# Optimization experiments

Hardware: AMD Instinct MI355X
Metric: run time of the kernel (lower is better)

The kernel has to match this reference:

```python
import jax, jax.numpy as jnp
import numpy as np

B, S, D, H, F = 8, 1024, 1024, 16, 4096
HD = D // H
SCALING = HD ** -0.5
EPS = 1e-5


def layer_norm(x, g, b):
    m = jnp.mean(x, axis=-1, keepdims=True)
    v = jnp.mean(jnp.square(x - m), axis=-1, keepdims=True)
    return (x - m) * jax.lax.rsqrt(v + EPS) * g + b


def setup_inputs() -> dict:
    key = jax.random.key(0)
    ks = jax.random.split(key, 8)
    std = 0.02
    return {
        "hidden_states": jax.random.normal(ks[0], (B, S, D), jnp.float32),
        "wq": jax.random.normal(ks[1], (D, D), jnp.float32) * std,
        "bq": jnp.zeros((D,), jnp.float32),
        "wk": jax.random.normal(ks[2], (D, D), jnp.float32) * std,
        "bk": jnp.zeros((D,), jnp.float32),
        "wv": jax.random.normal(ks[3], (D, D), jnp.float32) * std,
        "bv": jnp.zeros((D,), jnp.float32),
        "wo": jax.random.normal(ks[4], (D, D), jnp.float32) * std,
        "bo": jnp.zeros((D,), jnp.float32),
        "ln1_g": jnp.ones((D,), jnp.float32),
        "ln1_b": jnp.zeros((D,), jnp.float32),
        "fc1_w": jax.random.normal(ks[5], (F, D), jnp.float32) * std,
        "fc1_b": jnp.zeros((F,), jnp.float32),
        "fc2_w": jax.random.normal(ks[6], (D, F), jnp.float32) * std,
        "fc2_b": jnp.zeros((D,), jnp.float32),
        "ln2_g": jnp.ones((D,), jnp.float32),
        "ln2_b": jnp.zeros((D,), jnp.float32),
    }


def reference(hidden_states, wq, bq, wk, bk, wv, bv, wo, bo,
              ln1_g, ln1_b, fc1_w, fc1_b, fc2_w, fc2_b, ln2_g, ln2_b):
    hs = hidden_states
    residual = hs
    # --- manual multi-head self-attention (queries pre-scaled as in source) ---
    q = (hs @ wq.T + bq) * SCALING          # [B,S,D]
    k = hs @ wk.T + bk
    v = hs @ wv.T + bv
    q = q.reshape(B, S, H, HD).transpose(0, 2, 1, 3)  # [B,H,S,HD]
    k = k.reshape(B, S, H, HD).transpose(0, 2, 1, 3)
    v = v.reshape(B, S, H, HD).transpose(0, 2, 1, 3)
    scores = jnp.einsum("bhqd,bhkd->bhqk", q, k)      # [B,H,S,S]
    probs = jax.nn.softmax(scores, axis=-1)
    attn = jnp.einsum("bhqk,bhkd->bhqd", probs, v)    # [B,H,S,HD]
    attn = attn.transpose(0, 2, 1, 3).reshape(B, S, D)
    attn = attn @ wo.T + bo
    hs = layer_norm(residual + attn, ln1_g, ln1_b)
    # --- FFN ---
    residual = hs
    h = jax.nn.gelu(hs @ fc1_w.T + fc1_b, approximate=False)  # [B,S,F]
    h = h @ fc2_w.T + fc2_b
    hs = layer_norm(residual + h, ln2_g, ln2_b)
    return hs
```

## Files before the change

### kernel.cpp

```cpp
#include <hip/hip_runtime.h>
#include <hip/hip_bf16.h>
#include <math.h>

#define B_  8
#define S_  1024
#define D_  1024
#define H_  16
#define HD_ 64
#define F_  4096
#define NROWS_ (B_*S_)
#define SCALING_ 0.125f
#define EPS_ 1e-5f

typedef __attribute__((ext_vector_type(8))) short bf16x8;
typedef __attribute__((ext_vector_type(4))) float f32x4;
typedef __attribute__((ext_vector_type(4))) unsigned short us4;

__device__ __forceinline__ unsigned short f2bf(float f) {
    union { float f; unsigned int u; } x; x.f = f;
    unsigned int u = x.u;
    u += 0x7FFFu + ((u >> 16) & 1u);
    return (unsigned short)(u >> 16);
}

__device__ __forceinline__ f32x4 mfma16(bf16x8 a, bf16x8 b, f32x4 c) {
    return __builtin_amdgcn_mfma_f32_16x16x32_bf16(a, b, c, 0, 0, 0);
}

__device__ __forceinline__ void async_copy16(const unsigned short* g, unsigned short* l) {
    __builtin_amdgcn_global_load_lds(
        (const __attribute__((address_space(1))) void*)g,
        (__attribute__((address_space(3))) void*)l,
        16, 0, 0);
}

__device__ __forceinline__ bf16x8 ld_swz(const unsigned short* lds, int row, int k) {
    const int kg = (k >> 3) ^ (row & 7);
    return *reinterpret_cast<const bf16x8*>(lds + row * 64 + kg * 8);
}

__global__ __launch_bounds__(256)
void cvt_kernel(const float* __restrict__ in, unsigned short* __restrict__ out, int n4) {
    int i = blockIdx.x * 256 + threadIdx.x;
    if (i >= n4) return;
    const float4 v = reinterpret_cast<const float4*>(in)[i];
    us4 o = { f2bf(v.x), f2bf(v.y), f2bf(v.z), f2bf(v.w) };
    reinterpret_cast<us4*>(out)[i] = o;
}

template<int MODE>
__global__ __launch_bounds__(256)
void gemm_bt(const unsigned short* __restrict__ A,
             const unsigned short* __restrict__ Bw,
             const float* __restrict__ bias,
             const float* __restrict__ resid,
             float* __restrict__ outf,
             unsigned short* __restrict__ outb,
             float scale, int M, int N, int K)
{
    alignas(16) __shared__ unsigned short lA[128 * 64];
    alignas(16) __shared__ unsigned short lB[128 * 64];
    const int tid  = threadIdx.x;
    const int lane = tid & 63, wave = tid >> 6;
    const int wr = wave >> 1, wc = wave & 1;
    const int l15 = lane & 15, lg = lane >> 4;
    const int brow = blockIdx.y * 128, bcol = blockIdx.x * 128;

    f32x4 acc[4][4];
#pragma unroll
    for (int m = 0; m < 4; ++m)
#pragma unroll
        for (int n = 0; n < 4; ++n) acc[m][n] = f32x4{0.f, 0.f, 0.f, 0.f};

    for (int k0 = 0; k0 < K; k0 += 64) {
#pragma unroll
        for (int j = 0; j < 4; ++j) {
            const int c   = wave * 4 + j;
            const int p   = c * 64 + lane;
            const int row = p >> 3;
            const int kg  = (p & 7) ^ (row & 7);
            async_copy16(&A [(size_t)(brow + row) * K + k0 + kg * 8], &lA[c * 512]);
            async_copy16(&Bw[(size_t)(bcol + row) * K + k0 + kg * 8], &lB[c * 512]);
        }
        __syncthreads();
#pragma unroll
        for (int kk = 0; kk < 2; ++kk) {
            bf16x8 af[4], bfr[4];
#pragma unroll
            for (int m = 0; m < 4; ++m) af[m]  = ld_swz(lA, wr * 64 + m * 16 + l15, kk * 32 + lg * 8);
#pragma unroll
            for (int n = 0; n < 4; ++n) bfr[n] = ld_swz(lB, wc * 64 + n * 16 + l15, kk * 32 + lg * 8);
#pragma unroll
            for (int m = 0; m < 4; ++m)
#pragma unroll
                for (int n = 0; n < 4; ++n)
                    acc[m][n] = mfma16(af[m], bfr[n], acc[m][n]);
        }
        __syncthreads();
    }

#pragma unroll
    for (int m = 0; m < 4; ++m) {
#pragma unroll
        for (int n = 0; n < 4; ++n) {
#pragma unroll
            for (int r = 0; r < 4; ++r) {
                const int grow = brow + wr * 64 + m * 16 + lg * 4 + r;
                const int gcol = bcol + wc * 64 + n * 16 + l15;
                float v = acc[m][n][r] + bias[gcol];
                if constexpr (MODE == 0) {
                    v *= scale;
                    const int b = grow >> 10, s = grow & 1023, h = gcol >> 6, hd = gcol & 63;
                    outb[(((size_t)b * H_ + h) * S_ + s) * HD_ + hd] = f2bf(v);
                } else if constexpr (MODE == 1) {
                    const int b = grow >> 10, s = grow & 1023, h = gcol >> 6, hd = gcol & 63;
                    outb[(((size_t)b * H_ + h) * HD_ + hd) * S_ + s] = f2bf(v);
                } else if constexpr (MODE == 2 || MODE == 4) {
                    outf[(size_t)grow * N + gcol] = v + resid[(size_t)grow * N + gcol];
                } else {
                    float g = 0.5f * v * (1.0f + erff(v * 0.70710678118654752f));
                    outb[(size_t)grow * N + gcol] = f2bf(g);
                }
            }
        }
    }
}

__global__ __launch_bounds__(256)
void attn_kernel(const unsigned short* __restrict__ qb,
                 const unsigned short* __restrict__ kb,
                 const unsigned short* __restrict__ vtb,
                 unsigned short* __restrict__ attn)
{
    alignas(16) __shared__ unsigned short lK[64 * 64];
    alignas(16) __shared__ unsigned short lV[64 * 64];
    alignas(16) __shared__ unsigned short lP[4][16 * 72];
    const int bh = blockIdx.x, qblk = blockIdx.y;
    const int tid = threadIdx.x, lane = tid & 63, wave = tid >> 6;
    const int l15 = lane & 15, lg = lane >> 4;
    const int b = bh >> 4, h = bh & 15;

    const unsigned short* Kg = kb  + (size_t)bh * S_ * HD_;
    const unsigned short* Vg = vtb + (size_t)bh * HD_ * S_;
    const unsigned short* Qg = qb  + ((size_t)bh * S_ + qblk * 64 + wave * 16) * HD_;

    bf16x8 qf0 = *reinterpret_cast<const bf16x8*>(Qg + l15 * HD_ + lg * 8);
    bf16x8 qf1 = *reinterpret_cast<const bf16x8*>(Qg + l15 * HD_ + lg * 8 + 32);

    float mr[4], lr[4];
    f32x4 o[4];
#pragma unroll
    for (int r = 0; r < 4; ++r) { mr[r] = -1e30f; lr[r] = 0.f; }
#pragma unroll
    for (int n = 0; n < 4; ++n) o[n] = f32x4{0.f, 0.f, 0.f, 0.f};

    for (int t = 0; t < 16; ++t) {
#pragma unroll
        for (int j = 0; j < 2; ++j) {
            const int c   = wave * 2 + j;
            const int p   = c * 64 + lane;
            const int row = p >> 3;
            const int kg  = (p & 7) ^ (row & 7);
            async_copy16(&Kg[(size_t)(t * 64 + row) * HD_ + kg * 8], &lK[c * 512]);
            async_copy16(&Vg[(size_t)row * S_ + t * 64 + kg * 8],    &lV[c * 512]);
        }
        __syncthreads();

        f32x4 sf[4];
#pragma unroll
        for (int n = 0; n < 4; ++n) {
            f32x4 z = {0.f, 0.f, 0.f, 0.f};
            z     = mfma16(qf0, ld_swz(lK, n * 16 + l15, lg * 8), z);
            sf[n] = mfma16(qf1, ld_swz(lK, n * 16 + l15, 32 + lg * 8), z);
        }

        float tmax[4], corr[4], psum[4];
#pragma unroll
        for (int r = 0; r < 4; ++r)
            tmax[r] = fmaxf(fmaxf(sf[0][r], sf[1][r]), fmaxf(sf[2][r], sf[3][r]));
#pragma unroll
        for (int off = 1; off < 16; off <<= 1)
#pragma unroll
            for (int r = 0; r < 4; ++r) tmax[r] = fmaxf(tmax[r], __shfl_xor(tmax[r], off, 64));
#pragma unroll
        for (int r = 0; r < 4; ++r) {
            float mnew = fmaxf(mr[r], tmax[r]);
            corr[r] = __expf(mr[r] - mnew);
            mr[r] = mnew;
            psum[r] = 0.f;
        }
        unsigned short pbf[4][4];
#pragma unroll
        for (int n = 0; n < 4; ++n)
#pragma unroll
            for (int r = 0; r < 4; ++r) {
                float p = __expf(sf[n][r] - mr[r]);
                psum[r] += p;
                pbf[n][r] = f2bf(p);
            }
#pragma unroll
        for (int off = 1; off < 16; off <<= 1)
#pragma unroll
            for (int r = 0; r < 4; ++r) psum[r] += __shfl_xor(psum[r], off, 64);
#pragma unroll
        for (int r = 0; r < 4; ++r) lr[r] = lr[r] * corr[r] + psum[r];
#pragma unroll
        for (int n = 0; n < 4; ++n)
#pragma unroll
            for (int r = 0; r < 4; ++r) o[n][r] *= corr[r];

        unsigned short* Pl = &lP[wave][0];
#pragma unroll
        for (int n = 0; n < 4; ++n)
#pragma unroll
            for (int r = 0; r < 4; ++r)
                Pl[(lg * 4 + r) * 72 + n * 16 + l15] = pbf[n][r];
        asm volatile("s_waitcnt lgkmcnt(0)" ::: "memory");
        __builtin_amdgcn_sched_barrier(0);

#pragma unroll
        for (int kk = 0; kk < 2; ++kk) {
            bf16x8 pf = *reinterpret_cast<const bf16x8*>(Pl + l15 * 72 + kk * 32 + lg * 8);
#pragma unroll
            for (int n = 0; n < 4; ++n)
                o[n] = mfma16(pf, ld_swz(lV, n * 16 + l15, kk * 32 + lg * 8), o[n]);
        }
        __syncthreads();
    }

#pragma unroll
    for (int n = 0; n < 4; ++n)
#pragma unroll
        for (int r = 0; r < 4; ++r) {
            const int s = qblk * 64 + wave * 16 + lg * 4 + r;
            const int d = h * HD_ + n * 16 + l15;
            attn[((size_t)b * S_ + s) * D_ + d] = f2bf(o[n][r] / lr[r]);
        }
}

__global__ __launch_bounds__(256)
void ln_kernel(const float* __restrict__ in, const float* __restrict__ gam,
               const float* __restrict__ bet,
               float* __restrict__ outf, unsigned short* __restrict__ outbf)
{
    const int row = blockIdx.x, t = threadIdx.x;
    const float4 v = reinterpret_cast<const float4*>(in + (size_t)row * D_)[t];
    float s  = v.x + v.y + v.z + v.w;
    float s2 = v.x * v.x + v.y * v.y + v.z * v.z + v.w * v.w;
#pragma unroll
    for (int off = 32; off > 0; off >>= 1) {
        s  += __shfl_down(s, off, 64);
        s2 += __shfl_down(s2, off, 64);
    }
    __shared__ float red[2][4];
    if ((t & 63) == 0) { red[0][t >> 6] = s; red[1][t >> 6] = s2; }
    __syncthreads();
    s  = red[0][0] + red[0][1] + red[0][2] + red[0][3];
    s2 = red[1][0] + red[1][1] + red[1][2] + red[1][3];
    const float mean = s * (1.0f / D_);
    const float rstd = rsqrtf(s2 * (1.0f / D_) - mean * mean + EPS_);
    const float4 g4 = reinterpret_cast<const float4*>(gam)[t];
    const float4 b4 = reinterpret_cast<const float4*>(bet)[t];
    float4 y;
    y.x = (v.x - mean) * rstd * g4.x + b4.x;
    y.y = (v.y - mean) * rstd * g4.y + b4.y;
    y.z = (v.z - mean) * rstd * g4.z + b4.z;
    y.w = (v.w - mean) * rstd * g4.w + b4.w;
    if (outf)  reinterpret_cast<float4*>(outf + (size_t)row * D_)[t] = y;
    if (outbf) {
        us4 o = { f2bf(y.x), f2bf(y.y), f2bf(y.z), f2bf(y.w) };
        reinterpret_cast<us4*>(outbf + (size_t)row * D_)[t] = o;
    }
}

extern "C" void kernel_launch(void* const* d_in, const int* in_sizes, int n_in,
                              void* d_out, int out_size, void* d_ws, size_t ws_size,
                              hipStream_t stream)
{
    const float* hs   = (const float*)d_in[0];
    const float* wq   = (const float*)d_in[1];
    const float* bq   = (const float*)d_in[2];
    const float* wk   = (const float*)d_in[3];
    const float* bk   = (const float*)d_in[4];
    const float* wv   = (const float*)d_in[5];
    const float* bv   = (const float*)d_in[6];
    const float* wo   = (const float*)d_in[7];
    const float* bo   = (const float*)d_in[8];
    const float* ln1g = (const float*)d_in[9];
    const float* ln1b = (const float*)d_in[10];
    const float* fc1w = (const float*)d_in[11];
    const float* fc1b = (const float*)d_in[12];
    const float* fc2w = (const float*)d_in[13];
    const float* fc2b = (const float*)d_in[14];
    const float* ln2g = (const float*)d_in[15];
    const float* ln2b = (const float*)d_in[16];
    float* out = (float*)d_out;

    char* ws = (char*)d_ws;
    const size_t MB = 1024 * 1024;
    unsigned short* hs_bf = (unsigned short*)(ws + 0);
    unsigned short* wq_bf = (unsigned short*)(ws + 16 * MB);
    unsigned short* wk_bf = (unsigned short*)(ws + 18 * MB);
    unsigned short* wv_bf = (unsigned short*)(ws + 20 * MB);
    unsigned short* wo_bf = (unsigned short*)(ws + 22 * MB);
    unsigned short* f1_bf = (unsigned short*)(ws + 24 * MB);
    unsigned short* f2_bf = (unsigned short*)(ws + 32 * MB);
    unsigned short* qbf   = (unsigned short*)(ws + 40 * MB);
    unsigned short* kbf   = (unsigned short*)(ws + 56 * MB);
    unsigned short* vtbf  = (unsigned short*)(ws + 72 * MB);
    unsigned short* attnb = (unsigned short*)(ws + 88 * MB);
    float*          tmp   = (float*)(ws + 104 * MB);
    float*          ln1f  = (float*)(ws + 136 * MB);
    unsigned short* ln1bf = (unsigned short*)(ws + 168 * MB);
    unsigned short* h_bf  = (unsigned short*)(ws + 40 * MB);

    cvt_kernel<<<8192, 256, 0, stream>>>(hs,   hs_bf, 2097152);
    cvt_kernel<<<1024, 256, 0, stream>>>(wq,   wq_bf,  262144);
    cvt_kernel<<<1024, 256, 0, stream>>>(wk,   wk_bf,  262144);
    cvt_kernel<<<1024, 256, 0, stream>>>(wv,   wv_bf,  262144);
    cvt_kernel<<<1024, 256, 0, stream>>>(wo,   wo_bf,  262144);
    cvt_kernel<<<4096, 256, 0, stream>>>(fc1w, f1_bf, 1048576);
    cvt_kernel<<<4096, 256, 0, stream>>>(fc2w, f2_bf, 1048576);

    gemm_bt<0><<<dim3(8, 64),  256, 0, stream>>>(hs_bf, wq_bf, bq, nullptr, nullptr, qbf,  SCALING_, NROWS_, D_, D_);
    gemm_bt<0><<<dim3(8, 64),  256, 0, stream>>>(hs_bf, wk_bf, bk, nullptr, nullptr, kbf,  1.0f,     NROWS_, D_, D_);
    gemm_bt<1><<<dim3(8, 64),  256, 0, stream>>>(hs_bf, wv_bf, bv, nullptr, nullptr, vtbf, 1.0f,     NROWS_, D_, D_);
    attn_kernel<<<dim3(B_ * H_, S_ / 64), 256, 0, stream>>>(qbf, kbf, vtbf, attnb);
    gemm_bt<2><<<dim3(8, 64),  256, 0, stream>>>(attnb, wo_bf, bo, hs, tmp, nullptr, 1.0f, NROWS_, D_, D_);
    ln_kernel<<<NROWS_, 256, 0, stream>>>(tmp, ln1g, ln1b, ln1f, ln1bf);
    gemm_bt<3><<<dim3(32, 64), 256, 0, stream>>>(ln1bf, f1_bf, fc1b, nullptr, nullptr, h_bf, 1.0f, NROWS_, F_, D_);
    gemm_bt<4><<<dim3(8, 64),  256, 0, stream>>>(h_bf, f2_bf, fc2b, ln1f, tmp, nullptr, 1.0f, NROWS_, D_, F_);
    ln_kernel<<<NROWS_, 256, 0, stream>>>(tmp, ln2g, ln2b, out, nullptr);
    (void)in_sizes; (void)n_in; (void)out_size; (void)ws_size;
}
```

Before: 583.5 us.

## Double-buffer K/V tiles and transpose MFMA operands in attention kernel

The attention kernel now double-buffers the K and V tiles in LDS, issuing the async loads for the next tile before computing on the current one, and it drops one of the two barriers per iteration. The MFMA operands are swapped so each lane holds a full query row. That reduces the row-max and row-sum reductions to two cross-lane shuffles, lets P be written as packed bf16x4 stores, and makes the final output stores vectorized. The cost is twice the LDS for K/V, which may lower occupancy. The explicit lgkmcnt wait before re-reading P is also removed, so correctness depends on compiler-inserted waits.

```diff
diff --git a/kernel.cpp b/kernel.cpp
--- a/kernel.cpp
+++ b/kernel.cpp
@@ -21,6 +21,11 @@
     unsigned int u = x.u;
     u += 0x7FFFu + ((u >> 16) & 1u);
     return (unsigned short)(u >> 16);
+}
+
+__device__ __forceinline__ unsigned int pack_bf2(float a, float b) {
+    __hip_bfloat162 h = __float22bfloat162_rn(make_float2(a, b));
+    union { __hip_bfloat162 h; unsigned int u; } c; c.h = h; return c.u;
 }
 
 __device__ __forceinline__ f32x4 mfma16(bf16x8 a, bf16x8 b, f32x4 c) {
@@ -132,8 +137,8 @@
                  const unsigned short* __restrict__ vtb,
                  unsigned short* __restrict__ attn)
 {
-    alignas(16) __shared__ unsigned short lK[64 * 64];
-    alignas(16) __shared__ unsigned short lV[64 * 64];
+    alignas(16) __shared__ unsigned short lK[2][64 * 64];
+    alignas(16) __shared__ unsigned short lV[2][64 * 64];
     alignas(16) __shared__ unsigned short lP[4][16 * 72];
     const int bh = blockIdx.x, qblk = blockIdx.y;
     const int tid = threadIdx.x, lane = tid & 63, wave = tid >> 6;
@@ -147,95 +152,94 @@
     bf16x8 qf0 = *reinterpret_cast<const bf16x8*>(Qg + l15 * HD_ + lg * 8);
     bf16x8 qf1 = *reinterpret_cast<const bf16x8*>(Qg + l15 * HD_ + lg * 8 + 32);
 
-    float mr[4], lr[4];
+    float mr = -1e30f, lr = 0.f;
     f32x4 o[4];
 #pragma unroll
-    for (int r = 0; r < 4; ++r) { mr[r] = -1e30f; lr[r] = 0.f; }
-#pragma unroll
-    for (int n = 0; n < 4; ++n) o[n] = f32x4{0.f, 0.f, 0.f, 0.f};
+    for (int m = 0; m < 4; ++m) o[m] = f32x4{0.f, 0.f, 0.f, 0.f};
+
+#define STAGE(buf, t)                                                              \
+    {                                                                              \
+        _Pragma("unroll")                                                          \
+        for (int j = 0; j < 2; ++j) {                                              \
+            const int c   = wave * 2 + j;                      \
+            const int p   = c * 64 + lane;                 \
+            const int row = p >> 3;                                                \
+            const int kg  = (p & 7) ^ (row & 7);                                   \
+            async_copy16(&Kg[(size_t)((t) * 64 + row) * HD_ + kg * 8], &lK[buf][c * 512]); \
+            async_copy16(&Vg[(size_t)row * S_ + (t) * 64 + kg * 8],    &lV[buf][c * 512]); \
+        }                                                                          \
+    }
+
+    STAGE(0, 0);
+
+    unsigned short* Pl = &lP[wave][0];
 
     for (int t = 0; t < 16; ++t) {
-#pragma unroll
-        for (int j = 0; j < 2; ++j) {
-            const int c   = wave * 2 + j;
-            const int p   = c * 64 + lane;
-            const int row = p >> 3;
-            const int kg  = (p & 7) ^ (row & 7);
-            async_copy16(&Kg[(size_t)(t * 64 + row) * HD_ + kg * 8], &lK[c * 512]);
-            async_copy16(&Vg[(size_t)row * S_ + t * 64 + kg * 8],    &lV[c * 512]);
-        }
+        const int cur = t & 1;
         __syncthreads();
+        if (t < 15) STAGE(cur ^ 1, t + 1);
 
         f32x4 sf[4];
 #pragma unroll
         for (int n = 0; n < 4; ++n) {
             f32x4 z = {0.f, 0.f, 0.f, 0.f};
-            z     = mfma16(qf0, ld_swz(lK, n * 16 + l15, lg * 8), z);
-            sf[n] = mfma16(qf1, ld_swz(lK, n * 16 + l15, 32 + lg * 8), z);
-        }
-
-        float tmax[4], corr[4], psum[4];
-#pragma unroll
-        for (int r = 0; r < 4; ++r)
-            tmax[r] = fmaxf(fmaxf(sf[0][r], sf[1][r]), fmaxf(sf[2][r], sf[3][r]));
-#pragma unroll
-        for (int off = 1; off < 16; off <<= 1)
-#pragma unroll
-            for (int r = 0; r < 4; ++r) tmax[r] = fmaxf(tmax[r], __shfl_xor(tmax[r], off, 64));
-#pragma unroll
-        for (int r = 0; r < 4; ++r) {
-            float mnew = fmaxf(mr[r], tmax[r]);
-            corr[r] = __expf(mr[r] - mnew);
-            mr[r] = mnew;
-            psum[r] = 0.f;
-        }
-        unsigned short pbf[4][4];
+            z     = mfma16(ld_swz(lK[cur], n * 16 + l15, lg * 8),      qf0, z);
+            sf[n] = mfma16(ld_swz(lK[cur], n * 16 + l15, 32 + lg * 8), qf1, z);
+        }
+
+        float tmax = sf[0][0];
 #pragma unroll
         for (int n = 0; n < 4; ++n)
 #pragma unroll
-            for (int r = 0; r < 4; ++r) {
-                float p = __expf(sf[n][r] - mr[r]);
-                psum[r] += p;
-                pbf[n][r] = f2bf(p);
-            }
-#pragma unroll
-        for (int off = 1; off < 16; off <<= 1)
-#pragma unroll
-            for (int r = 0; r < 4; ++r) psum[r] += __shfl_xor(psum[r], off, 64);
-#pragma unroll
-        for (int r = 0; r < 4; ++r) lr[r] = lr[r] * corr[r] + psum[r];
+            for (int r = 0; r < 4; ++r) tmax = fmaxf(tmax, sf[n][r]);
+        tmax = fmaxf(tmax, __shfl_xor(tmax, 16, 64));
+        tmax = fmaxf(tmax, __shfl_xor(tmax, 32, 64));
+        const float mnew = fmaxf(mr, tmax);
+        const float corr = __expf(mr - mnew);
+        mr = mnew;
+
+        float ps = 0.f;
+        uint2 pk[4];
+#pragma unroll
+        for (int n = 0; n < 4; ++n) {
+            float p0 = __expf(sf[n][0] - mr);
+            float p1 = __expf(sf[n][1] - mr);
+            float p2 = __expf(sf[n][2] - mr);
+            float p3 = __expf(sf[n][3] - mr);
+            ps += (p0 + p1) + (p2 + p3);
+            pk[n].x = pack_bf2(p0, p1);
+            pk[n].y = pack_bf2(p2, p3);
+        }
+        ps += __shfl_xor(ps, 16, 64);
+        ps += __shfl_xor(ps, 32, 64);
+        lr = lr * corr + ps;
+#pragma unroll
+        for (int m = 0; m < 4; ++m)
+#pragma unroll
+            for (int r = 0; r < 4; ++r) o[m][r] *= corr;
+
 #pragma unroll
         for (int n = 0; n < 4; ++n)
-#pragma unroll
-            for (int r = 0; r < 4; ++r) o[n][r] *= corr[r];
-
-        unsigned short* Pl = &lP[wave][0];
-#pragma unroll
-        for (int n = 0; n < 4; ++n)
-#pragma unroll
-            for (int r = 0; r < 4; ++r)
-                Pl[(lg * 4 + r) * 72 + n * 16 + l15] = pbf[n][r];
-        asm volatile("s_waitcnt lgkmcnt(0)" ::: "memory");
-        __builtin_amdgcn_sched_barrier(0);
+            *reinterpret_cast<uint2*>(Pl + l15 * 72 + n * 16 + lg * 4) = pk[n];
 
 #pragma unroll
         for (int kk = 0; kk < 2; ++kk) {
             bf16x8 pf = *reinterpret_cast<const bf16x8*>(Pl + l15 * 72 + kk * 32 + lg * 8);
 #pragma unroll
-            for (int n = 0; n < 4; ++n)
-                o[n] = mfma16(pf, ld_swz(lV, n * 16 + l15, kk * 32 + lg * 8), o[n]);
-        }
-        __syncthreads();
-    }
-
-#pragma unroll
-    for (int n = 0; n < 4; ++n)
-#pragma unroll
-        for (int r = 0; r < 4; ++r) {
-            const int s = qblk * 64 + wave * 16 + lg * 4 + r;
-            const int d = h * HD_ + n * 16 + l15;
-            attn[((size_t)b * S_ + s) * D_ + d] = f2bf(o[n][r] / lr[r]);
-        }
+            for (int m = 0; m < 4; ++m)
+                o[m] = mfma16(ld_swz(lV[cur], m * 16 + l15, kk * 32 + lg * 8), pf, o[m]);
+        }
+    }
+#undef STAGE
+
+    const int s = qblk * 64 + wave * 16 + l15;
+    const float rinv = 1.0f / lr;
+#pragma unroll
+    for (int m = 0; m < 4; ++m) {
+        us4 w = { f2bf(o[m][0] * rinv), f2bf(o[m][1] * rinv),
+                  f2bf(o[m][2] * rinv), f2bf(o[m][3] * rinv) };
+        *reinterpret_cast<us4*>(attn + ((size_t)b * S_ + s) * D_ + h * HD_ + m * 16 + lg * 4) = w;
+    }
 }
 
 __global__ __launch_bounds__(256)
```

Result: faster. 565.6 us (-3.1%).
